# Kernel tuning notes

Hardware: AMD Instinct MI355X
Metric: run time of the kernel (lower is better)

Reference implementation:

```python
import jax, jax.numpy as jnp
import numpy as np

DIM_IN = 768
DIM_OUT = 64
SEQ = 4096
BATCH = 4

def setup_inputs() -> dict:
    key = jax.random.key(0)
    ks = jax.random.split(key, 7)
    s = 1.0 / np.sqrt(DIM_IN)
    return {
        "x": jax.random.normal(ks[0], (BATCH, SEQ, DIM_IN), dtype=jnp.float32),
        "wq": jax.random.uniform(ks[1], (DIM_IN, DIM_OUT), jnp.float32, -s, s),
        "bq": jax.random.uniform(ks[2], (DIM_OUT,), jnp.float32, -s, s),
        "wk": jax.random.uniform(ks[3], (DIM_IN, DIM_OUT), jnp.float32, -s, s),
        "bk": jax.random.uniform(ks[4], (DIM_OUT,), jnp.float32, -s, s),
        "wv": jax.random.uniform(ks[5], (DIM_IN, DIM_OUT), jnp.float32, -s, s),
        "bv": jax.random.uniform(ks[6], (DIM_OUT,), jnp.float32, -s, s),
    }

def reference(x, wq, bq, wk, bk, wv, bv):
    # QKV projections: (B, S, D_in) @ (D_in, D_out) + bias
    q = x @ wq + bq
    k = x @ wk + bk
    v = x @ wv + bv
    # full causal attention, scores scaled by sqrt(d_out) AFTER masking (as in source)
    scores = jnp.einsum('bqd,bkd->bqk', q, k)  # (B, S, S)
    seq = x.shape[1]
    causal = jnp.tril(jnp.ones((seq, seq), dtype=bool))  # True = keep
    scores = jnp.where(causal, scores, -jnp.inf)
    scale = 1.0 / np.sqrt(k.shape[-1]).astype(np.float32)
    weights = jax.nn.softmax(scores * scale, axis=-1)
    # dropout_rate = 0.0 -> identity
    return jnp.einsum('bqk,bkd->bqd', weights, v)
```

## Files before the change

kernel.cpp:

```cpp
#include <hip/hip_runtime.h>
#include <hip/hip_bf16.h>

#define BATCH 4
#define SEQ   4096
#define DIN   768
#define DOUT  64

typedef __attribute__((ext_vector_type(4))) float f32x4;
typedef __attribute__((ext_vector_type(8))) short short8;
typedef __attribute__((ext_vector_type(4))) short short4v;

#define QSCALE 0.18033688011112043f

static __device__ __forceinline__ unsigned short f2bf(float f) {
    union { float f; unsigned u; } un; un.f = f;
    unsigned r = un.u + 0x7FFF + ((un.u >> 16) & 1);
    return (unsigned short)(r >> 16);
}
static __device__ __forceinline__ float bf2f(unsigned short h) {
    union { unsigned u; float f; } un; un.u = ((unsigned)h) << 16;
    return un.f;
}

__global__ void wprep_kernel(const float* __restrict__ wq,
                             const float* __restrict__ wk,
                             const float* __restrict__ wv,
                             unsigned short* __restrict__ wF) {
    __shared__ float lds[64][65];
    int o = blockIdx.x / 12, kt = blockIdx.x % 12;
    const float* w = (o == 0) ? wq : (o == 1) ? wk : wv;
    int tid = threadIdx.x;
    int k0 = kt * 64;
    #pragma unroll
    for (int i = 0; i < 16; ++i) {
        int flat = tid + i * 256;
        int kl = flat >> 6, n = flat & 63;
        lds[kl][n] = w[(k0 + kl) * 64 + n];
    }
    __syncthreads();
    int lane = tid & 63;
    int m = lane & 15, g = lane >> 4;
    #pragma unroll
    for (int i = 0; i < 2; ++i) {
        int f = i * 4 + (tid >> 6);
        int t = f >> 1, kcl = f & 1;
        int kc = kt * 2 + kcl;
        int nc = o * 4 + t;
        short8 v;
        #pragma unroll
        for (int j = 0; j < 8; ++j)
            v[j] = (short)f2bf(lds[kcl * 32 + g * 8 + j][t * 16 + m]);
        *(short8*)&wF[(size_t)(nc * 24 + kc) * 512 + lane * 8] = v;
    }
}

__global__ void __launch_bounds__(256) proj_kernel(
        const float* __restrict__ x,
        const float* __restrict__ bq,
        const float* __restrict__ bk,
        const float* __restrict__ bv,
        const unsigned short* __restrict__ wF,
        unsigned short* __restrict__ Qf,
        unsigned short* __restrict__ Kf,
        unsigned short* __restrict__ Vf) {
    __shared__ __align__(16) unsigned short xs[32][776];
    __shared__ unsigned short tr[4][16][24];

    int tid = threadIdx.x;
    int w = tid >> 6;
    int lane = tid & 63;
    int m = lane & 15, g = lane >> 4;
    int r0 = blockIdx.x * 32;

    {
        const float* xbase = x + (size_t)r0 * DIN;
        #pragma unroll
        for (int i = 0; i < 24; ++i) {
            int flat4 = tid + i * 256;
            int row = flat4 / 192;
            int c4 = flat4 - row * 192;
            float4 v = *(const float4*)(xbase + (size_t)row * DIN + c4 * 4);
            short4v sv;
            sv[0] = (short)f2bf(v.x); sv[1] = (short)f2bf(v.y);
            sv[2] = (short)f2bf(v.z); sv[3] = (short)f2bf(v.w);
            *(short4v*)&xs[row][c4 * 4] = sv;
        }
    }
    __syncthreads();

    f32x4 acc[2][3];
    #pragma unroll
    for (int st = 0; st < 2; ++st)
        #pragma unroll
        for (int t = 0; t < 3; ++t) acc[st][t] = (f32x4){0.f, 0.f, 0.f, 0.f};

    for (int kc = 0; kc < 24; ++kc) {
        short8 af0 = *(const short8*)&xs[m][kc * 32 + g * 8];
        short8 af1 = *(const short8*)&xs[16 + m][kc * 32 + g * 8];
        #pragma unroll
        for (int tt = 0; tt < 3; ++tt) {
            int nc = w * 3 + tt;
            short8 bfrg = *(const short8*)(wF + (size_t)(nc * 24 + kc) * 512 + lane * 8);
            acc[0][tt] = __builtin_amdgcn_mfma_f32_16x16x32_bf16(af0, bfrg, acc[0][tt], 0, 0, 0);
            acc[1][tt] = __builtin_amdgcn_mfma_f32_16x16x32_bf16(af1, bfrg, acc[1][tt], 0, 0, 0);
        }
    }

    int b2 = r0 >> 12;
    int s = (r0 & 4095) >> 5;
    #pragma unroll
    for (int st = 0; st < 2; ++st) {
        #pragma unroll
        for (int tt = 0; tt < 3; ++tt) {
            int nc = w * 3 + tt;
            int o = nc >> 2;
            int t = nc & 3;
            const float* bias_p = (o == 0) ? bq : (o == 1) ? bk : bv;
            float bias = bias_p[t * 16 + m];
            #pragma unroll
            for (int r = 0; r < 4; ++r) {
                float val = acc[st][tt][r] + bias;
                if (o == 0) val *= QSCALE;
                tr[w][g * 4 + r][m] = f2bf(val);
            }
            if (o < 2) {
                if (g < 2) {
                    short8 v8;
                    #pragma unroll
                    for (int j = 0; j < 8; ++j) v8[j] = (short)tr[w][m][g * 8 + j];
                    unsigned short* dst = (o == 0) ? Qf : Kf;
                    int c = t >> 1;
                    *(short8*)&dst[(size_t)((blockIdx.x * 2 + st) * 2 + c) * 512
                                   + (((t & 1) * 2 + g) * 16 + m) * 8] = v8;
                }
            } else {
                if (g < 2) {
                    short8 v8;
                    #pragma unroll
                    for (int j = 0; j < 8; ++j) v8[j] = (short)tr[w][g * 8 + j][m];
                    *(short8*)&Vf[((size_t)(b2 * 128 + s) * 4 + t) * 512
                                  + ((st * 2 + g) * 16 + m) * 8] = v8;
                }
            }
        }
    }
}

__global__ void __launch_bounds__(512, 1) attn_kernel(
        const unsigned short* __restrict__ Qf,
        const unsigned short* __restrict__ Kf,
        const unsigned short* __restrict__ Vf,
        float* __restrict__ out) {
    __shared__ __align__(16) unsigned short P_lds[8][32][36];
    __shared__ __align__(16) unsigned short pacc[8][16][68];
    __shared__ float pm[8][16];
    __shared__ float pl[8][16];

    int j = blockIdx.x;
    int b = j & 3;
    int qt = j >> 2;
    int base0 = qt * 16;
    int base1 = (255 - qt) * 16;
    int ns0 = (qt + 2) >> 1;
    int ns1 = (257 - qt) >> 1;
    int tid = threadIdx.x;
    int w = tid >> 6;
    int lane = tid & 63;
    int m = lane & 15, g = lane >> 4;

    const unsigned short* Q0 = Qf + (size_t)(b * 256 + qt) * 1024 + lane * 8;
    const unsigned short* Q1 = Qf + (size_t)(b * 256 + 255 - qt) * 1024 + lane * 8;
    short8 qf[2][2];
    qf[0][0] = *(const short8*)(Q0);
    qf[0][1] = *(const short8*)(Q0 + 512);
    qf[1][0] = *(const short8*)(Q1);
    qf[1][1] = *(const short8*)(Q1 + 512);

    short8 onesB = (short8){0,0,0,0,0,0,0,0};
    if (m == 0) {
        #pragma unroll
        for (int jj = 0; jj < 8; ++jj) onesB[jj] = (short)0x3F80;
    }

    f32x4 acc[2][5];
    #pragma unroll
    for (int rt = 0; rt < 2; ++rt)
        #pragma unroll
        for (int t = 0; t < 5; ++t) acc[rt][t] = (f32x4){0.f, 0.f, 0.f, 0.f};
    float mrun[2][4];
    #pragma unroll
    for (int rt = 0; rt < 2; ++rt)
        #pragma unroll
        for (int r = 0; r < 4; ++r) mrun[rt][r] = -INFINITY;

    const unsigned short* Kbase = Kf + (size_t)(b * 256) * 1024 + lane * 8;
    const unsigned short* Vbase = Vf + (size_t)(b * 128) * 2048 + lane * 8;

    short8 kf[4], vf[4];
    if (w < ns1) {
        #pragma unroll
        for (int t = 0; t < 4; ++t) {
            kf[t] = *(const short8*)(Kbase + (size_t)w * 2048 + t * 512);
            vf[t] = *(const short8*)(Vbase + (size_t)w * 2048 + t * 512);
        }
    }

    for (int s = w; s < ns1; s += 8) {
        int kv0 = s * 32;
        int sn = s + 8;
        short8 kn[4], vn[4];
        if (sn < ns1) {
            #pragma unroll
            for (int t = 0; t < 4; ++t) {
                kn[t] = *(const short8*)(Kbase + (size_t)sn * 2048 + t * 512);
                vn[t] = *(const short8*)(Vbase + (size_t)sn * 2048 + t * 512);
            }
        }

        #pragma unroll
        for (int rt = 0; rt < 2; ++rt) {
            if (rt == 0 && s >= ns0) continue;
            int qbase = (rt == 0) ? base0 : base1;
            bool lastd = (s == ((rt == 0) ? ns0 : ns1) - 1);

            f32x4 sc[2];
            sc[0] = (f32x4){0.f, 0.f, 0.f, 0.f};
            sc[1] = (f32x4){0.f, 0.f, 0.f, 0.f};
            sc[0] = __builtin_amdgcn_mfma_f32_16x16x32_bf16(qf[rt][0], kf[0], sc[0], 0, 0, 0);
            sc[0] = __builtin_amdgcn_mfma_f32_16x16x32_bf16(qf[rt][1], kf[1], sc[0], 0, 0, 0);
            sc[1] = __builtin_amdgcn_mfma_f32_16x16x32_bf16(qf[rt][0], kf[2], sc[1], 0, 0, 0);
            sc[1] = __builtin_amdgcn_mfma_f32_16x16x32_bf16(qf[rt][1], kf[3], sc[1], 0, 0, 0);

            if (lastd) {
                #pragma unroll
                for (int tt = 0; tt < 2; ++tt)
                    #pragma unroll
                    for (int r = 0; r < 4; ++r)
                        if (kv0 + tt * 16 + m > qbase + g * 4 + r) sc[tt][r] = -INFINITY;
            }

            bool need = false;
            #pragma unroll
            for (int r = 0; r < 4; ++r) {
                float th = mrun[rt][r] + 8.0f;
                need = need | (sc[0][r] > th) | (sc[1][r] > th);
            }
            if (__any(need)) {
                float rmax[4];
                #pragma unroll
                for (int r = 0; r < 4; ++r) rmax[r] = fmaxf(sc[0][r], sc[1][r]);
                #pragma unroll
                for (int msk = 1; msk <= 8; msk <<= 1)
                    #pragma unroll
                    for (int r = 0; r < 4; ++r)
                        rmax[r] = fmaxf(rmax[r], __shfl_xor(rmax[r], msk));
                #pragma unroll
                for (int r = 0; r < 4; ++r) {
                    float mnew = fmaxf(mrun[rt][r], rmax[r]);
                    float alpha = __builtin_amdgcn_exp2f(mrun[rt][r] - mnew);
                    mrun[rt][r] = mnew;
                    #pragma unroll
                    for (int t = 0; t < 5; ++t) acc[rt][t][r] *= alpha;
                }
            }

            #pragma unroll
            for (int tt = 0; tt < 2; ++tt)
                #pragma unroll
                for (int r = 0; r < 4; ++r)
                    P_lds[w][rt * 16 + g * 4 + r][tt * 16 + m] =
                        f2bf(__builtin_amdgcn_exp2f(sc[tt][r] - mrun[rt][r]));
            short8 pa = *(const short8*)&P_lds[w][rt * 16 + m][g * 8];

            #pragma unroll
            for (int t = 0; t < 4; ++t)
                acc[rt][t] = __builtin_amdgcn_mfma_f32_16x16x32_bf16(pa, vf[t], acc[rt][t], 0, 0, 0);
            acc[rt][4] = __builtin_amdgcn_mfma_f32_16x16x32_bf16(pa, onesB, acc[rt][4], 0, 0, 0);
        }

        if (sn < ns1) {
            #pragma unroll
            for (int t = 0; t < 4; ++t) { kf[t] = kn[t]; vf[t] = vn[t]; }
        }
    }

    #pragma unroll
    for (int rt = 0; rt < 2; ++rt) {
        int qbase = (rt == 0) ? base0 : base1;
        if (m == 0) {
            #pragma unroll
            for (int r = 0; r < 4; ++r) {
                pm[w][g * 4 + r] = mrun[rt][r];
                pl[w][g * 4 + r] = acc[rt][4][r];
            }
        }
        #pragma unroll
        for (int t = 0; t < 4; ++t)
            #pragma unroll
            for (int r = 0; r < 4; ++r)
                pacc[w][g * 4 + r][t * 16 + m] = f2bf(acc[rt][t][r]);
        __syncthreads();

        if (tid < 256) {
            int row = tid >> 4;
            int c4 = (tid & 15) * 4;
            float mmax = pm[0][row];
            #pragma unroll
            for (int w2 = 1; w2 < 8; ++w2) mmax = fmaxf(mmax, pm[w2][row]);
            float lt = 0.f;
            float o0 = 0.f, o1 = 0.f, o2 = 0.f, o3 = 0.f;
            #pragma unroll
            for (int w2 = 0; w2 < 8; ++w2) {
                float sc2 = __builtin_amdgcn_exp2f(pm[w2][row] - mmax);
                lt += pl[w2][row] * sc2;
                short4v pa4 = *(const short4v*)&pacc[w2][row][c4];
                o0 += bf2f((unsigned short)pa4[0]) * sc2;
                o1 += bf2f((unsigned short)pa4[1]) * sc2;
                o2 += bf2f((unsigned short)pa4[2]) * sc2;
                o3 += bf2f((unsigned short)pa4[3]) * sc2;
            }
            float invl = 1.0f / lt;
            float4 res = make_float4(o0 * invl, o1 * invl, o2 * invl, o3 * invl);
            *(float4*)&out[(size_t)(b * SEQ + qbase + row) * DOUT + c4] = res;
        }
        __syncthreads();
    }
}

extern "C" void kernel_launch(void* const* d_in, const int* in_sizes, int n_in,
                              void* d_out, int out_size, void* d_ws, size_t ws_size,
                              hipStream_t stream) {
    const float* x  = (const float*)d_in[0];
    const float* wq = (const float*)d_in[1];
    const float* bq = (const float*)d_in[2];
    const float* wk = (const float*)d_in[3];
    const float* bk = (const float*)d_in[4];
    const float* wv = (const float*)d_in[5];
    const float* bv = (const float*)d_in[6];
    float* out = (float*)d_out;

    char* ws = (char*)d_ws;
    unsigned short* wF = (unsigned short*)ws;
    unsigned short* Qf = (unsigned short*)(ws + 294912);
    unsigned short* Kf = (unsigned short*)(ws + 294912 + 2097152);
    unsigned short* Vf = (unsigned short*)(ws + 294912 + 4194304);

    wprep_kernel<<<36, 256, 0, stream>>>(wq, wk, wv, wF);
    proj_kernel<<<512, 256, 0, stream>>>(x, bq, bk, bv, wF, Qf, Kf, Vf);
    attn_kernel<<<512, 512, 0, stream>>>(Qf, Kf, Vf, out);
}
```

Before: 56.85 us.

## Compute transposed scores to keep P in registers, drop LDS round-trip

Scores are now computed as K·Q^T, so each lane holds a single query column. The softmax max and sum reduce with two cross-lane shuffles instead of four, and the row sum is accumulated in registers, which removes the extra MFMA against a ones matrix. P is packed to bf16 and redistributed with lane shuffles in place of the per-wave LDS store and reload. K/V prefetch is split and moved between the MFMAs, and launch bounds are raised to two blocks per CU. Register pressure under the tighter bound may cause spills, and the shuffle-based P transpose adds ds_bpermute traffic.

```diff
diff --git a/kernel.cpp b/kernel.cpp
--- a/kernel.cpp
+++ b/kernel.cpp
@@ -20,6 +20,9 @@
 static __device__ __forceinline__ float bf2f(unsigned short h) {
     union { unsigned u; float f; } un; un.u = ((unsigned)h) << 16;
     return un.f;
+}
+static __device__ __forceinline__ unsigned packbf(float lo, float hi) {
+    return ((unsigned)f2bf(hi) << 16) | (unsigned)f2bf(lo);
 }
 
 __global__ void wprep_kernel(const float* __restrict__ wq,
@@ -146,12 +149,11 @@
     }
 }
 
-__global__ void __launch_bounds__(512, 1) attn_kernel(
+__global__ void __launch_bounds__(512, 2) attn_kernel(
         const unsigned short* __restrict__ Qf,
         const unsigned short* __restrict__ Kf,
         const unsigned short* __restrict__ Vf,
         float* __restrict__ out) {
-    __shared__ __align__(16) unsigned short P_lds[8][32][36];
     __shared__ __align__(16) unsigned short pacc[8][16][68];
     __shared__ float pm[8][16];
     __shared__ float pl[8][16];
@@ -170,31 +172,25 @@
 
     const unsigned short* Q0 = Qf + (size_t)(b * 256 + qt) * 1024 + lane * 8;
     const unsigned short* Q1 = Qf + (size_t)(b * 256 + 255 - qt) * 1024 + lane * 8;
-    short8 qf[2][2];
-    qf[0][0] = *(const short8*)(Q0);
-    qf[0][1] = *(const short8*)(Q0 + 512);
-    qf[1][0] = *(const short8*)(Q1);
-    qf[1][1] = *(const short8*)(Q1 + 512);
-
-    short8 onesB = (short8){0,0,0,0,0,0,0,0};
-    if (m == 0) {
-        #pragma unroll
-        for (int jj = 0; jj < 8; ++jj) onesB[jj] = (short)0x3F80;
-    }
-
-    f32x4 acc[2][5];
+    short8 qf00 = *(const short8*)(Q0);
+    short8 qf01 = *(const short8*)(Q0 + 512);
+    short8 qf10 = *(const short8*)(Q1);
+    short8 qf11 = *(const short8*)(Q1 + 512);
+
+    f32x4 acc[2][4];
     #pragma unroll
     for (int rt = 0; rt < 2; ++rt)
         #pragma unroll
-        for (int t = 0; t < 5; ++t) acc[rt][t] = (f32x4){0.f, 0.f, 0.f, 0.f};
-    float mrun[2][4];
-    #pragma unroll
-    for (int rt = 0; rt < 2; ++rt)
-        #pragma unroll
-        for (int r = 0; r < 4; ++r) mrun[rt][r] = -INFINITY;
+        for (int t = 0; t < 4; ++t) acc[rt][t] = (f32x4){0.f, 0.f, 0.f, 0.f};
+    float mrun0 = -INFINITY, mrun1 = -INFINITY;
+    float lsum0 = 0.f, lsum1 = 0.f;
 
     const unsigned short* Kbase = Kf + (size_t)(b * 256) * 1024 + lane * 8;
     const unsigned short* Vbase = Vf + (size_t)(b * 128) * 2048 + lane * 8;
+
+    int srcA = m + 16 * ((g & 1) * 2);
+    int srcB = srcA + 16;
+    bool hi = (g >= 2);
 
     short8 kf[4], vf[4];
     if (w < ns1) {
@@ -208,97 +204,153 @@
     for (int s = w; s < ns1; s += 8) {
         int kv0 = s * 32;
         int sn = s + 8;
-        short8 kn[4], vn[4];
-        if (sn < ns1) {
-            #pragma unroll
-            for (int t = 0; t < 4; ++t) {
-                kn[t] = *(const short8*)(Kbase + (size_t)sn * 2048 + t * 512);
-                vn[t] = *(const short8*)(Vbase + (size_t)sn * 2048 + t * 512);
-            }
-        }
-
-        #pragma unroll
-        for (int rt = 0; rt < 2; ++rt) {
-            if (rt == 0 && s >= ns0) continue;
-            int qbase = (rt == 0) ? base0 : base1;
-            bool lastd = (s == ((rt == 0) ? ns0 : ns1) - 1);
-
-            f32x4 sc[2];
-            sc[0] = (f32x4){0.f, 0.f, 0.f, 0.f};
-            sc[1] = (f32x4){0.f, 0.f, 0.f, 0.f};
-            sc[0] = __builtin_amdgcn_mfma_f32_16x16x32_bf16(qf[rt][0], kf[0], sc[0], 0, 0, 0);
-            sc[0] = __builtin_amdgcn_mfma_f32_16x16x32_bf16(qf[rt][1], kf[1], sc[0], 0, 0, 0);
-            sc[1] = __builtin_amdgcn_mfma_f32_16x16x32_bf16(qf[rt][0], kf[2], sc[1], 0, 0, 0);
-            sc[1] = __builtin_amdgcn_mfma_f32_16x16x32_bf16(qf[rt][1], kf[3], sc[1], 0, 0, 0);
-
-            if (lastd) {
-                #pragma unroll
-                for (int tt = 0; tt < 2; ++tt)
+        bool have = (sn < ns1);
+        bool do0 = (s < ns0);
+
+        if (do0) {
+            f32x4 st0 = (f32x4){0.f, 0.f, 0.f, 0.f};
+            f32x4 st1 = (f32x4){0.f, 0.f, 0.f, 0.f};
+            st0 = __builtin_amdgcn_mfma_f32_16x16x32_bf16(kf[0], qf00, st0, 0, 0, 0);
+            st0 = __builtin_amdgcn_mfma_f32_16x16x32_bf16(kf[1], qf01, st0, 0, 0, 0);
+            st1 = __builtin_amdgcn_mfma_f32_16x16x32_bf16(kf[2], qf00, st1, 0, 0, 0);
+            st1 = __builtin_amdgcn_mfma_f32_16x16x32_bf16(kf[3], qf01, st1, 0, 0, 0);
+            if (s == ns0 - 1) {
+                int q = base0 + m;
+                #pragma unroll
+                for (int r = 0; r < 4; ++r) {
+                    if (kv0 + g * 4 + r > q)      st0[r] = -INFINITY;
+                    if (kv0 + 16 + g * 4 + r > q) st1[r] = -INFINITY;
+                }
+            }
+            float th = mrun0 + 8.0f;
+            bool need = (st0[0] > th) | (st0[1] > th) | (st0[2] > th) | (st0[3] > th)
+                      | (st1[0] > th) | (st1[1] > th) | (st1[2] > th) | (st1[3] > th);
+            if (__any(need)) {
+                float rmax = fmaxf(fmaxf(fmaxf(st0[0], st0[1]), fmaxf(st0[2], st0[3])),
+                                   fmaxf(fmaxf(st1[0], st1[1]), fmaxf(st1[2], st1[3])));
+                rmax = fmaxf(rmax, __shfl_xor(rmax, 16));
+                rmax = fmaxf(rmax, __shfl_xor(rmax, 32));
+                float mnew = fmaxf(mrun0, rmax);
+                float alpha = __builtin_amdgcn_exp2f(mrun0 - mnew);
+                mrun0 = mnew;
+                lsum0 *= alpha;
+                #pragma unroll
+                for (int t = 0; t < 4; ++t)
                     #pragma unroll
-                    for (int r = 0; r < 4; ++r)
-                        if (kv0 + tt * 16 + m > qbase + g * 4 + r) sc[tt][r] = -INFINITY;
-            }
-
-            bool need = false;
-            #pragma unroll
-            for (int r = 0; r < 4; ++r) {
-                float th = mrun[rt][r] + 8.0f;
-                need = need | (sc[0][r] > th) | (sc[1][r] > th);
-            }
+                    for (int r = 0; r < 4; ++r) acc[0][t][r] *= alpha;
+            }
+            float p00 = __builtin_amdgcn_exp2f(st0[0] - mrun0);
+            float p01 = __builtin_amdgcn_exp2f(st0[1] - mrun0);
+            float p02 = __builtin_amdgcn_exp2f(st0[2] - mrun0);
+            float p03 = __builtin_amdgcn_exp2f(st0[3] - mrun0);
+            float p10 = __builtin_amdgcn_exp2f(st1[0] - mrun0);
+            float p11 = __builtin_amdgcn_exp2f(st1[1] - mrun0);
+            float p12 = __builtin_amdgcn_exp2f(st1[2] - mrun0);
+            float p13 = __builtin_amdgcn_exp2f(st1[3] - mrun0);
+            float ssum = ((p00 + p01) + (p02 + p03)) + ((p10 + p11) + (p12 + p13));
+            ssum += __shfl_xor(ssum, 16);
+            ssum += __shfl_xor(ssum, 32);
+            lsum0 += ssum;
+            unsigned d0 = packbf(p00, p01), d1 = packbf(p02, p03);
+            unsigned d2 = packbf(p10, p11), d3 = packbf(p12, p13);
+            unsigned a0 = __shfl(d0, srcA), a1 = __shfl(d1, srcA);
+            unsigned a2 = __shfl(d2, srcA), a3 = __shfl(d3, srcA);
+            unsigned b0 = __shfl(d0, srcB), b1 = __shfl(d1, srcB);
+            unsigned b2 = __shfl(d2, srcB), b3 = __shfl(d3, srcB);
+            union { unsigned u[4]; short8 s8; } pb;
+            pb.u[0] = hi ? a2 : a0; pb.u[1] = hi ? a3 : a1;
+            pb.u[2] = hi ? b2 : b0; pb.u[3] = hi ? b3 : b1;
+            #pragma unroll
+            for (int t = 0; t < 4; ++t)
+                acc[0][t] = __builtin_amdgcn_mfma_f32_16x16x32_bf16(vf[t], pb.s8, acc[0][t], 0, 0, 0);
+        }
+
+        {
+            f32x4 st0 = (f32x4){0.f, 0.f, 0.f, 0.f};
+            f32x4 st1 = (f32x4){0.f, 0.f, 0.f, 0.f};
+            st0 = __builtin_amdgcn_mfma_f32_16x16x32_bf16(kf[0], qf10, st0, 0, 0, 0);
+            st0 = __builtin_amdgcn_mfma_f32_16x16x32_bf16(kf[1], qf11, st0, 0, 0, 0);
+            st1 = __builtin_amdgcn_mfma_f32_16x16x32_bf16(kf[2], qf10, st1, 0, 0, 0);
+            st1 = __builtin_amdgcn_mfma_f32_16x16x32_bf16(kf[3], qf11, st1, 0, 0, 0);
+
+            if (have) {
+                #pragma unroll
+                for (int t = 0; t < 4; ++t)
+                    kf[t] = *(const short8*)(Kbase + (size_t)sn * 2048 + t * 512);
+            }
+
+            if (s == ns1 - 1) {
+                int q = base1 + m;
+                #pragma unroll
+                for (int r = 0; r < 4; ++r) {
+                    if (kv0 + g * 4 + r > q)      st0[r] = -INFINITY;
+                    if (kv0 + 16 + g * 4 + r > q) st1[r] = -INFINITY;
+                }
+            }
+            float th = mrun1 + 8.0f;
+            bool need = (st0[0] > th) | (st0[1] > th) | (st0[2] > th) | (st0[3] > th)
+                      | (st1[0] > th) | (st1[1] > th) | (st1[2] > th) | (st1[3] > th);
             if (__any(need)) {
-                float rmax[4];
-                #pragma unroll
-                for (int r = 0; r < 4; ++r) rmax[r] = fmaxf(sc[0][r], sc[1][r]);
-                #pragma unroll
-                for (int msk = 1; msk <= 8; msk <<= 1)
+                float rmax = fmaxf(fmaxf(fmaxf(st0[0], st0[1]), fmaxf(st0[2], st0[3])),
+                                   fmaxf(fmaxf(st1[0], st1[1]), fmaxf(st1[2], st1[3])));
+                rmax = fmaxf(rmax, __shfl_xor(rmax, 16));
+                rmax = fmaxf(rmax, __shfl_xor(rmax, 32));
+                float mnew = fmaxf(mrun1, rmax);
+                float alpha = __builtin_amdgcn_exp2f(mrun1 - mnew);
+                mrun1 = mnew;
+                lsum1 *= alpha;
+                #pragma unroll
+                for (int t = 0; t < 4; ++t)
                     #pragma unroll
-                    for (int r = 0; r < 4; ++r)
-                        rmax[r] = fmaxf(rmax[r], __shfl_xor(rmax[r], msk));
-                #pragma unroll
-                for (int r = 0; r < 4; ++r) {
-                    float mnew = fmaxf(mrun[rt][r], rmax[r]);
-                    float alpha = __builtin_amdgcn_exp2f(mrun[rt][r] - mnew);
-                    mrun[rt][r] = mnew;
-                    #pragma unroll
-                    for (int t = 0; t < 5; ++t) acc[rt][t][r] *= alpha;
-                }
-            }
-
-            #pragma unroll
-            for (int tt = 0; tt < 2; ++tt)
-                #pragma unroll
-                for (int r = 0; r < 4; ++r)
-                    P_lds[w][rt * 16 + g * 4 + r][tt * 16 + m] =
-                        f2bf(__builtin_amdgcn_exp2f(sc[tt][r] - mrun[rt][r]));
-            short8 pa = *(const short8*)&P_lds[w][rt * 16 + m][g * 8];
-
+                    for (int r = 0; r < 4; ++r) acc[1][t][r] *= alpha;
+            }
+            float p00 = __builtin_amdgcn_exp2f(st0[0] - mrun1);
+            float p01 = __builtin_amdgcn_exp2f(st0[1] - mrun1);
+            float p02 = __builtin_amdgcn_exp2f(st0[2] - mrun1);
+            float p03 = __builtin_amdgcn_exp2f(st0[3] - mrun1);
+            float p10 = __builtin_amdgcn_exp2f(st1[0] - mrun1);
+            float p11 = __builtin_amdgcn_exp2f(st1[1] - mrun1);
+            float p12 = __builtin_amdgcn_exp2f(st1[2] - mrun1);
+            float p13 = __builtin_amdgcn_exp2f(st1[3] - mrun1);
+            float ssum = ((p00 + p01) + (p02 + p03)) + ((p10 + p11) + (p12 + p13));
+            ssum += __shfl_xor(ssum, 16);
+            ssum += __shfl_xor(ssum, 32);
+            lsum1 += ssum;
+            unsigned d0 = packbf(p00, p01), d1 = packbf(p02, p03);
+            unsigned d2 = packbf(p10, p11), d3 = packbf(p12, p13);
+            unsigned a0 = __shfl(d0, srcA), a1 = __shfl(d1, srcA);
+            unsigned a2 = __shfl(d2, srcA), a3 = __shfl(d3, srcA);
+            unsigned b0 = __shfl(d0, srcB), b1 = __shfl(d1, srcB);
+            unsigned b2 = __shfl(d2, srcB), b3 = __shfl(d3, srcB);
+            union { unsigned u[4]; short8 s8; } pb;
+            pb.u[0] = hi ? a2 : a0; pb.u[1] = hi ? a3 : a1;
+            pb.u[2] = hi ? b2 : b0; pb.u[3] = hi ? b3 : b1;
             #pragma unroll
             for (int t = 0; t < 4; ++t)
-                acc[rt][t] = __builtin_amdgcn_mfma_f32_16x16x32_bf16(pa, vf[t], acc[rt][t], 0, 0, 0);
-            acc[rt][4] = __builtin_amdgcn_mfma_f32_16x16x32_bf16(pa, onesB, acc[rt][4], 0, 0, 0);
-        }
-
-        if (sn < ns1) {
-            #pragma unroll
-            for (int t = 0; t < 4; ++t) { kf[t] = kn[t]; vf[t] = vn[t]; }
+                acc[1][t] = __builtin_amdgcn_mfma_f32_16x16x32_bf16(vf[t], pb.s8, acc[1][t], 0, 0, 0);
+
+            if (have) {
+                #pragma unroll
+                for (int t = 0; t < 4; ++t)
+                    vf[t] = *(const short8*)(Vbase + (size_t)sn * 2048 + t * 512);
+            }
         }
     }
 
     #pragma unroll
     for (int rt = 0; rt < 2; ++rt) {
         int qbase = (rt == 0) ? base0 : base1;
-        if (m == 0) {
-            #pragma unroll
-            for (int r = 0; r < 4; ++r) {
-                pm[w][g * 4 + r] = mrun[rt][r];
-                pl[w][g * 4 + r] = acc[rt][4][r];
-            }
+        float mr = (rt == 0) ? mrun0 : mrun1;
+        float ls = (rt == 0) ? lsum0 : lsum1;
+        if (lane < 16) {
+            pm[w][m] = mr;
+            pl[w][m] = ls;
         }
         #pragma unroll
         for (int t = 0; t < 4; ++t)
             #pragma unroll
             for (int r = 0; r < 4; ++r)
-                pacc[w][g * 4 + r][t * 16 + m] = f2bf(acc[rt][t][r]);
+                pacc[w][m][t * 16 + g * 4 + r] = f2bf(acc[rt][t][r]);
         __syncthreads();
 
         if (tid < 256) {
```

Result: faster. 49.47 us (-13.0%).
